# Kernel tuning notes

Hardware: AMD Instinct MI355X
Metric: run time of the kernel (lower is better)

The kernel has to match this reference:

```python
import jax, jax.numpy as jnp
import numpy as np

B, T, H = 4, 2048, 1024
N, D = 16, 64  # heads, key_dim (= value_dim)
SCALE = 1.0 / float(D) ** 0.5


def setup_inputs() -> dict:
    key = jax.random.key(0)
    ks = jax.random.split(key, 10)
    s = 0.02
    return {
        "query": jax.random.normal(ks[0], (B, T, H), jnp.float32),
        "value": jax.random.normal(ks[1], (B, T, H), jnp.float32),
        "Wq": jax.random.normal(ks[2], (N * D, H), jnp.float32) * s,
        "bq": jnp.zeros((N * D,), jnp.float32),
        "Wk": jax.random.normal(ks[3], (N * D, H), jnp.float32) * s,
        "bk": jnp.zeros((N * D,), jnp.float32),
        "Wv": jax.random.normal(ks[4], (N * D, H), jnp.float32) * s,
        "bv": jnp.zeros((N * D,), jnp.float32),
        "Wo": jax.random.normal(ks[5], (H, N * D), jnp.float32) * s,
        "bo": jnp.zeros((H,), jnp.float32),
    }


def reference(query, value, Wq, bq, Wk, bk, Wv, bv, Wo, bo):
    key_in = value  # key=None path: key = value
    q = (query @ Wq.T + bq).reshape(B, -1, N, D)   # [B,T,N,D]
    k = (key_in @ Wk.T + bk).reshape(B, -1, N, D)  # [B,S,N,D]
    v = (value @ Wv.T + bv).reshape(B, -1, N, D)   # [B,S,N,D]
    # scores [T,S,B,N], softmax over S (axis=1), scaled dot-product
    scores = jnp.einsum('btnd,bsnd->tsbn', q, k) * SCALE
    attn = jax.nn.softmax(scores, axis=1)
    # output [B,T,N,D]
    out = jnp.einsum('tsbn,bsnd->btnd', attn, v)
    out = out.reshape(B, T, N * D)
    return out @ Wo.T + bo
```

## Files before the change

### kernel.cpp

```cpp
#include <hip/hip_runtime.h>
#include <cstdint>
#include <cstddef>

typedef unsigned short u16;
typedef __bf16 bf16x8 __attribute__((ext_vector_type(8)));
typedef __bf16 bf16x2 __attribute__((ext_vector_type(2)));
typedef float f32x4 __attribute__((ext_vector_type(4)));
typedef float f32x16 __attribute__((ext_vector_type(16)));

#define B_   4
#define T_   2048
#define H_   1024
#define NH_  16
#define DH_  64
#define M_   (B_ * T_)
#define KDIM 1024
#define QSCALE 0.18033688011112042f

#define BM 128
#define BN 128
#define BK 32

__device__ __forceinline__ u16 f2bf(float f) {
    unsigned u = __float_as_uint(f);
    unsigned r = (u + 0x7fffu + ((u >> 16) & 1u)) >> 16;
    return (u16)r;
}

__device__ __forceinline__ unsigned packbf2(float a, float b) {
    bf16x2 v = { (__bf16)a, (__bf16)b };
    return __builtin_bit_cast(unsigned, v);
}

__device__ __forceinline__ float exp2_fast(float x) {
#if __has_builtin(__builtin_amdgcn_exp2f)
    return __builtin_amdgcn_exp2f(x);
#else
    return exp2f(x);
#endif
}

__device__ __forceinline__ void plswap(unsigned &a, unsigned &b) {
#if __has_builtin(__builtin_amdgcn_permlane32_swap)
    auto r = __builtin_amdgcn_permlane32_swap(a, b, false, false);
    a = (unsigned)r[0]; b = (unsigned)r[1];
#else
    int hi = (threadIdx.x & 32);
    unsigned x = (unsigned)__shfl_xor((int)(hi ? b : a), 32);
    unsigned na = hi ? x : a;
    unsigned nb = hi ? b : x;
    a = na; b = nb;
#endif
}

__device__ __forceinline__ void gload16(const void* g, void* l) {
    __builtin_amdgcn_global_load_lds(
        (const __attribute__((address_space(1))) unsigned int*)g,
        (__attribute__((address_space(3))) unsigned int*)l,
        16, 0, 0);
}

__device__ __forceinline__ f32x16 mfma32(bf16x8 a, bf16x8 b, f32x16 c) {
    return __builtin_amdgcn_mfma_f32_32x32x16_bf16(a, b, c, 0, 0, 0);
}

__global__ __launch_bounds__(256) void f2bf_hex(
    const float* s0, u16* d0, int n0, const float* s1, u16* d1, int n1,
    const float* s2, u16* d2, int n2, const float* s3, u16* d3, int n3,
    const float* s4, u16* d4, int n4j, const float* s5, u16* d5, int n5)
{
    const float* s; u16* d; int n;
    switch (blockIdx.y) {
        case 0: s = s0; d = d0; n = n0; break;
        case 1: s = s1; d = d1; n = n1; break;
        case 2: s = s2; d = d2; n = n2; break;
        case 3: s = s3; d = d3; n = n3; break;
        case 4: s = s4; d = d4; n = n4j; break;
        default: s = s5; d = d5; n = n5; break;
    }
    int i = blockIdx.x * blockDim.x + threadIdx.x;
    int stride = gridDim.x * blockDim.x;
    for (; i < n; i += stride) {
        float4 f = reinterpret_cast<const float4*>(s)[i];
        ushort4 o;
        o.x = f2bf(f.x); o.y = f2bf(f.y); o.z = f2bf(f.z); o.w = f2bf(f.w);
        reinterpret_cast<ushort4*>(d)[i] = o;
    }
}

__device__ __forceinline__ void gemm_core(
    const u16* __restrict__ X, const u16* __restrict__ W,
    const float* __restrict__ bias,
    u16* __restrict__ dst_bf, float* __restrict__ dst_f,
    float scale, int mode, int r0, int c0)
{
    __shared__ u16 lds[17408];
    char* ldsA = (char*)lds;
    char* ldsB = (char*)lds + 8192;

    const int tid = threadIdx.x;
    const int wid = tid >> 6;
    const int l15 = tid & 15;
    const int l4  = (tid & 63) >> 4;
    const int wr = wid >> 1, wc = wid & 1;

    const u16* gA = X + (size_t)(r0 + (tid >> 2)) * KDIM + (tid & 3) * 8;
    const u16* gB = W + (size_t)(c0 + (tid >> 2)) * KDIM + (tid & 3) * 8;
    char* sA0 = ldsA + wid * 1024;
    char* sA1 = ldsA + 4096 + wid * 1024;
    char* sB0 = ldsB + wid * 1024;
    char* sB1 = ldsB + 4096 + wid * 1024;

    f32x4 acc[4][4];
#pragma unroll
    for (int m = 0; m < 4; ++m)
#pragma unroll
        for (int n = 0; n < 4; ++n) acc[m][n] = (f32x4){0.f, 0.f, 0.f, 0.f};

    gload16(gA, sA0); gload16(gA + 64 * KDIM, sA1);
    gload16(gB, sB0); gload16(gB + 64 * KDIM, sB1);

    const int arow = wr * 64 + l15;
    const int brow = wc * 64 + l15;

    for (int kt = 0; kt < KDIM / BK; ++kt) {
        __syncthreads();
        bf16x8 a[4], b[4];
#pragma unroll
        for (int m = 0; m < 4; ++m)
            a[m] = *(const bf16x8*)(ldsA + (arow + m * 16) * 64 + l4 * 16);
#pragma unroll
        for (int n = 0; n < 4; ++n)
            b[n] = *(const bf16x8*)(ldsB + (brow + n * 16) * 64 + l4 * 16);
#pragma unroll
        for (int m = 0; m < 4; ++m)
#pragma unroll
            for (int n = 0; n < 4; ++n)
                acc[m][n] = __builtin_amdgcn_mfma_f32_16x16x32_bf16(a[m], b[n], acc[m][n], 0, 0, 0);
        __syncthreads();
        if (kt + 1 < KDIM / BK) {
            const u16* pa = gA + (kt + 1) * BK;
            const u16* pb = gB + (kt + 1) * BK;
            gload16(pa, sA0); gload16(pa + 64 * KDIM, sA1);
            gload16(pb, sB0); gload16(pb + 64 * KDIM, sB1);
        }
    }

    if (mode == 2) {
#pragma unroll
        for (int m = 0; m < 4; ++m)
#pragma unroll
            for (int n = 0; n < 4; ++n) {
                int cg = c0 + wc * 64 + n * 16 + l15;
                float bv = bias[cg];
                int rg = r0 + wr * 64 + m * 16 + l4 * 4;
#pragma unroll
                for (int j = 0; j < 4; ++j)
                    dst_f[(size_t)(rg + j) * H_ + cg] = acc[m][n][j] + bv;
            }
    } else if (mode == 0) {
        __syncthreads();
        u16 (*ldsR)[136] = (u16(*)[136])lds;
#pragma unroll
        for (int m = 0; m < 4; ++m)
#pragma unroll
            for (int n = 0; n < 4; ++n) {
                int cl = wc * 64 + n * 16 + l15;
                float bv = bias[c0 + cl];
                int rl = wr * 64 + m * 16 + l4 * 4;
#pragma unroll
                for (int j = 0; j < 4; ++j)
                    ldsR[rl + j][cl] = f2bf((acc[m][n][j] + bv) * scale);
            }
        __syncthreads();
        int b2 = r0 >> 11, tb = r0 & (T_ - 1);
#pragma unroll
        for (int it = 0; it < 8; ++it) {
            int id = tid + it * 256;
            int row = id >> 4;
            int ch = id & 15;
            int head = (c0 >> 6) + (ch >> 3);
            int d0 = (ch & 7) * 8;
            uint4 v = *(const uint4*)&ldsR[row][ch * 8];
            *(uint4*)&dst_bf[(((size_t)(b2 * NH_ + head) * T_ + tb + row) << 6) + d0] = v;
        }
    } else {
        __syncthreads();
        u16 (*ldsT)[136] = (u16(*)[136])lds;
#pragma unroll
        for (int m = 0; m < 4; ++m)
#pragma unroll
            for (int n = 0; n < 4; ++n) {
                int cl = wc * 64 + n * 16 + l15;
                float bv = bias[c0 + cl];
                int rl = wr * 64 + m * 16 + l4 * 4;
#pragma unroll
                for (int j = 0; j < 4; ++j)
                    ldsT[cl][rl + j] = f2bf(acc[m][n][j] + bv);
            }
        __syncthreads();
        int b = r0 >> 11, tb = r0 & (T_ - 1);
#pragma unroll
        for (int it = 0; it < 8; ++it) {
            int chunk = tid + it * 256;
            int cl = chunk >> 4;
            int r8 = (chunk & 15) << 3;
            int cg = c0 + cl;
            int head = cg >> 6, d = cg & 63;
            uint4 v = *(const uint4*)&ldsT[cl][r8];
            *(uint4*)&dst_bf[((size_t)((b * NH_ + head) * DH_ + d) * T_) + tb + r8] = v;
        }
    }
}

__global__ __launch_bounds__(256) void gemm_qkv(
    const u16* __restrict__ qbf, const u16* __restrict__ vbf,
    const u16* __restrict__ Wqb, const u16* __restrict__ Wkb, const u16* __restrict__ Wvb,
    const float* __restrict__ bq, const float* __restrict__ bk, const float* __restrict__ bv,
    u16* __restrict__ Qd, u16* __restrict__ Kd, u16* __restrict__ Vtd)
{
    const int orig = blockIdx.y * 24 + blockIdx.x;
    const int swz = (orig & 7) * 192 + (orig >> 3);
    const int bx = swz % 24;
    const int by = swz / 24;
    const int seg = bx >> 3;
    const int r0 = by * BM;
    const int c0 = (bx & 7) * BN;

    if (seg == 0)
        gemm_core(qbf, Wqb, bq, Qd, nullptr, QSCALE, 0, r0, c0);
    else if (seg == 1)
        gemm_core(vbf, Wkb, bk, Kd, nullptr, 1.0f, 0, r0, c0);
    else
        gemm_core(vbf, Wvb, bv, Vtd, nullptr, 1.0f, 1, r0, c0);
}

__global__ __launch_bounds__(256) void gemm_out(
    const u16* __restrict__ AO, const u16* __restrict__ Wob,
    const float* __restrict__ bo, float* __restrict__ out)
{
    const int orig = blockIdx.y * 8 + blockIdx.x;
    const int swz = (orig & 7) * 64 + (orig >> 3);
    const int bx = swz & 7;
    const int by = swz >> 3;
    gemm_core(AO, Wob, bo, nullptr, out, 1.0f, 2, by * BM, bx * BN);
}

#define KVB 64

__global__ __launch_bounds__(256, 2) void attn64(
    const u16* __restrict__ Q, const u16* __restrict__ K,
    const u16* __restrict__ Vt, u16* __restrict__ AO)
{
    __shared__ u16 lds[16384];
    char* const base = (char*)lds;

    const int tid = threadIdx.x;
    const int wid = tid >> 6;
    const int lane = tid & 63;
    const int l31 = lane & 31;
    const int hi = lane >> 5;

    const int orig = blockIdx.y * 8 + blockIdx.x;
    const int swz = (orig & 7) * 64 + (orig >> 3);
    const int bn = swz >> 3;
    const int q0w = (swz & 7) * 256 + wid * 64;
    const int b = bn >> 4, head = bn & 15;

    const u16* Qb = Q + ((size_t)bn * T_ + q0w + l31) * DH_;
    const u16* Kb = K + (size_t)bn * T_ * DH_;
    const u16* Vb = Vt + (size_t)bn * DH_ * T_;

    bf16x8 qfa[4], qfb[4];
#pragma unroll
    for (int c = 0; c < 4; ++c) {
        qfa[c] = *(const bf16x8*)(Qb + c * 16 + hi * 8);
        qfb[c] = *(const bf16x8*)(Qb + 32 * DH_ + c * 16 + hi * 8);
    }

    bf16x8 ones;
#pragma unroll
    for (int e = 0; e < 8; ++e) ones[e] = (__bf16)1.0f;

    f32x16 accO00, accO01, accO10, accO11, La, Lb;
#pragma unroll
    for (int r = 0; r < 16; ++r) {
        accO00[r] = 0.f; accO01[r] = 0.f;
        accO10[r] = 0.f; accO11[r] = 0.f;
        La[r] = 0.f; Lb[r] = 0.f;
    }

    const int srow = tid >> 3;
    const int scsw = (tid & 7) ^ (srow & 7);
    const int rowsw = l31 & 7;

    const u16* kSrc = Kb + (size_t)srow * DH_ + scsw * 8;
    const u16* vSrc = Vb + (size_t)srow * T_ + scsw * 8;

#define STAGE(dK, dV) do { \
    gload16(kSrc,            (dK) + tid * 16); \
    gload16(kSrc + 32 * DH_, (dK) + 4096 + tid * 16); \
    gload16(vSrc,            (dV) + tid * 16); \
    gload16(vSrc + 32 * T_,  (dV) + 4096 + tid * 16); \
    kSrc += KVB * DH_; vSrc += KVB; } while (0)

    char* const kb0 = base;
    char* const vb0 = base + 8192;
    char* const kb1 = base + 16384;
    char* const vb1 = base + 24576;

    auto process = [&](const char* kc, const char* vc) {
        f32x16 sA0, sA1, sB0, sB1;
#pragma unroll
        for (int r = 0; r < 16; ++r) { sA0[r] = 0.f; sA1[r] = 0.f; sB0[r] = 0.f; sB1[r] = 0.f; }
        __builtin_amdgcn_s_setprio(1);
#pragma unroll
        for (int c = 0; c < 4; ++c) {
            const int c16 = ((2 * c + hi) ^ rowsw) * 16;
            bf16x8 k0 = *(const bf16x8*)(kc + l31 * 128 + c16);
            bf16x8 k1 = *(const bf16x8*)(kc + 4096 + l31 * 128 + c16);
            sA0 = mfma32(k0, qfa[c], sA0);
            sA1 = mfma32(k1, qfa[c], sA1);
            sB0 = mfma32(k0, qfb[c], sB0);
            sB1 = mfma32(k1, qfb[c], sB1);
        }
        __builtin_amdgcn_s_setprio(0);

#pragma unroll
        for (int r = 0; r < 16; ++r) {
            sA0[r] = exp2_fast(sA0[r]);
            sA1[r] = exp2_fast(sA1[r]);
            sB0[r] = exp2_fast(sB0[r]);
            sB1[r] = exp2_fast(sB1[r]);
        }

        unsigned w0a[8], w1a[8], w0b[8], w1b[8];
#pragma unroll
        for (int k2 = 0; k2 < 8; ++k2) {
            w0a[k2] = packbf2(sA0[2 * k2], sA0[2 * k2 + 1]);
            w1a[k2] = packbf2(sA1[2 * k2], sA1[2 * k2 + 1]);
            w0b[k2] = packbf2(sB0[2 * k2], sB0[2 * k2 + 1]);
            w1b[k2] = packbf2(sB1[2 * k2], sB1[2 * k2 + 1]);
        }
        plswap(w0a[0], w0a[2]); plswap(w0a[1], w0a[3]);
        plswap(w0a[4], w0a[6]); plswap(w0a[5], w0a[7]);
        plswap(w1a[0], w1a[2]); plswap(w1a[1], w1a[3]);
        plswap(w1a[4], w1a[6]); plswap(w1a[5], w1a[7]);
        plswap(w0b[0], w0b[2]); plswap(w0b[1], w0b[3]);
        plswap(w0b[4], w0b[6]); plswap(w0b[5], w0b[7]);
        plswap(w1b[0], w1b[2]); plswap(w1b[1], w1b[3]);
        plswap(w1b[4], w1b[6]); plswap(w1b[5], w1b[7]);

        __builtin_amdgcn_s_setprio(1);
#pragma unroll
        for (int ks = 0; ks < 4; ++ks) {
            union { unsigned w[4]; bf16x8 v; } pa, pb;
            const unsigned* sa_ = (ks < 2) ? w0a : w1a;
            const unsigned* sb_ = (ks < 2) ? w0b : w1b;
            const int o = (ks & 1) * 4;
            pa.w[0] = sa_[o + 0]; pa.w[1] = sa_[o + 1];
            pa.w[2] = sa_[o + 2]; pa.w[3] = sa_[o + 3];
            pb.w[0] = sb_[o + 0]; pb.w[1] = sb_[o + 1];
            pb.w[2] = sb_[o + 2]; pb.w[3] = sb_[o + 3];
            const int c16 = ((2 * ks + hi) ^ rowsw) * 16;
            bf16x8 v0f = *(const bf16x8*)(vc + l31 * 128 + c16);
            bf16x8 v1f = *(const bf16x8*)(vc + 4096 + l31 * 128 + c16);
            accO00 = mfma32(v0f, pa.v, accO00);
            accO01 = mfma32(v1f, pa.v, accO01);
            accO10 = mfma32(v0f, pb.v, accO10);
            accO11 = mfma32(v1f, pb.v, accO11);
            La = mfma32(ones, pa.v, La);
            Lb = mfma32(ones, pb.v, Lb);
        }
        __builtin_amdgcn_s_setprio(0);
    };

    STAGE(kb0, vb0);
    __syncthreads();

    for (int it = 0; it < T_ / KVB; it += 2) {
        STAGE(kb1, vb1);
        process(kb0, vb0);
        __syncthreads();
        if (it + 2 < T_ / KVB) STAGE(kb0, vb0);
        process(kb1, vb1);
        __syncthreads();
    }

    char* myO = base + wid * 8192;
    float inva = 1.f / La[0];
    float invb = 1.f / Lb[0];
#pragma unroll
    for (int n = 0; n < 2; ++n)
#pragma unroll
        for (int r = 0; r < 16; ++r) {
            int d = n * 32 + (r & 3) + 8 * (r >> 2) + 4 * hi;
            int c16 = (d >> 3) ^ rowsw;
            float va = (n == 0 ? accO00[r] : accO01[r]) * inva;
            float vb2 = (n == 0 ? accO10[r] : accO11[r]) * invb;
            *(u16*)(myO + l31 * 128 + c16 * 16 + (d & 7) * 2) = f2bf(va);
            *(u16*)(myO + (32 + l31) * 128 + c16 * 16 + (d & 7) * 2) = f2bf(vb2);
        }
    asm volatile("s_waitcnt lgkmcnt(0)" ::: "memory");
#pragma unroll
    for (int it = 0; it < 8; ++it) {
        int id = lane + it * 64;
        int row = id >> 3;
        int c = id & 7;
        int c16s = c ^ (row & 7);
        uint4 val = *(const uint4*)(myO + row * 128 + c16s * 16);
        *(uint4*)&AO[(size_t)(b * T_ + q0w + row) * (NH_ * DH_) + head * DH_ + c * 8] = val;
    }
#undef STAGE
}

extern "C" void kernel_launch(void* const* d_in, const int* in_sizes, int n_in,
                              void* d_out, int out_size, void* d_ws, size_t ws_size,
                              hipStream_t stream)
{
    const float* query = (const float*)d_in[0];
    const float* value = (const float*)d_in[1];
    const float* Wq = (const float*)d_in[2];
    const float* bq = (const float*)d_in[3];
    const float* Wk = (const float*)d_in[4];
    const float* bk = (const float*)d_in[5];
    const float* Wv = (const float*)d_in[6];
    const float* bv = (const float*)d_in[7];
    const float* Wo = (const float*)d_in[8];
    const float* bo = (const float*)d_in[9];
    float* out = (float*)d_out;

    u16* ws = (u16*)d_ws;
    const size_t E8M = (size_t)8 << 20;
    u16* qbf = ws;
    u16* vbf = ws + E8M;
    u16* Wqb = ws + 2 * E8M;
    u16* Wkb = Wqb + (1u << 20);
    u16* Wvb = Wkb + (1u << 20);
    u16* Wob = Wvb + (1u << 20);
    u16* Qd  = Wob + (1u << 20);
    u16* Kd  = Qd + E8M;
    u16* Vtd = Kd + E8M;
    u16* AO  = Vtd + E8M;

    const int nBig = (B_ * T_ * H_) / 4;
    const int nW   = (KDIM * KDIM) / 4;
    f2bf_hex<<<dim3(512, 6), 256, 0, stream>>>(
        query, qbf, nBig, value, vbf, nBig,
        Wq, Wqb, nW, Wk, Wkb, nW, Wv, Wvb, nW, Wo, Wob, nW);

    gemm_qkv<<<dim3(24, 64), 256, 0, stream>>>(qbf, vbf, Wqb, Wkb, Wvb,
                                               bq, bk, bv, Qd, Kd, Vtd);

    attn64<<<dim3(8, 64), 256, 0, stream>>>(Qd, Kd, Vtd, AO);

    gemm_out<<<dim3(8, 64), 256, 0, stream>>>(AO, Wob, bo, out);
}
```

Before: 196.8 us.

## Double-buffer GEMM LDS, widen attention KV tile, compute softmax denominator on VALU

The shared GEMM core now keeps two LDS buffers. It prefetches the next K-slice before computing on the current one, which leaves one vmcnt wait plus barrier per step instead of two __syncthreads. The attention kernel loads 128 keys per stage instead of 64, with a wider swizzled V layout and double the LDS (64 KB per block). Each stage is processed as two 64-key halves. The row-sum of probabilities, previously done with extra MFMAs against a vector of ones, is now accumulated in fp32 on the VALU and reduced across the two half-waves at the end, which frees matrix-core cycles at the cost of more VALU adds and higher LDS pressure per block.

```diff
diff --git a/kernel.cpp b/kernel.cpp
--- a/kernel.cpp
+++ b/kernel.cpp
@@ -64,6 +64,10 @@
     return __builtin_amdgcn_mfma_f32_32x32x16_bf16(a, b, c, 0, 0, 0);
 }
 
+__device__ __forceinline__ void wait_barrier() {
+    asm volatile("s_waitcnt vmcnt(0)\n\ts_barrier" ::: "memory");
+}
+
 __global__ __launch_bounds__(256) void f2bf_hex(
     const float* s0, u16* d0, int n0, const float* s1, u16* d1, int n1,
     const float* s2, u16* d2, int n2, const float* s3, u16* d3, int n3,
@@ -95,8 +99,7 @@
     float scale, int mode, int r0, int c0)
 {
     __shared__ u16 lds[17408];
-    char* ldsA = (char*)lds;
-    char* ldsB = (char*)lds + 8192;
+    char* const base = (char*)lds;
 
     const int tid = threadIdx.x;
     const int wid = tid >> 6;
@@ -106,45 +109,45 @@
 
     const u16* gA = X + (size_t)(r0 + (tid >> 2)) * KDIM + (tid & 3) * 8;
     const u16* gB = W + (size_t)(c0 + (tid >> 2)) * KDIM + (tid & 3) * 8;
-    char* sA0 = ldsA + wid * 1024;
-    char* sA1 = ldsA + 4096 + wid * 1024;
-    char* sB0 = ldsB + wid * 1024;
-    char* sB1 = ldsB + 4096 + wid * 1024;
 
     f32x4 acc[4][4];
 #pragma unroll
     for (int m = 0; m < 4; ++m)
 #pragma unroll
         for (int n = 0; n < 4; ++n) acc[m][n] = (f32x4){0.f, 0.f, 0.f, 0.f};
-
-    gload16(gA, sA0); gload16(gA + 64 * KDIM, sA1);
-    gload16(gB, sB0); gload16(gB + 64 * KDIM, sB1);
 
     const int arow = wr * 64 + l15;
     const int brow = wc * 64 + l15;
 
+#define STAGEG(p, kt) do { \
+    const u16* pa_ = gA + (kt) * BK; \
+    const u16* pb_ = gB + (kt) * BK; \
+    char* dA_ = base + (p) * 16384 + wid * 1024; \
+    char* dB_ = dA_ + 8192; \
+    gload16(pa_, dA_); gload16(pa_ + 64 * KDIM, dA_ + 4096); \
+    gload16(pb_, dB_); gload16(pb_ + 64 * KDIM, dB_ + 4096); } while (0)
+
+    STAGEG(0, 0);
+    wait_barrier();
+
     for (int kt = 0; kt < KDIM / BK; ++kt) {
-        __syncthreads();
+        if (kt + 1 < KDIM / BK) STAGEG((kt + 1) & 1, kt + 1);
+        const char* bufp = base + (kt & 1) * 16384;
         bf16x8 a[4], b[4];
 #pragma unroll
         for (int m = 0; m < 4; ++m)
-            a[m] = *(const bf16x8*)(ldsA + (arow + m * 16) * 64 + l4 * 16);
+            a[m] = *(const bf16x8*)(bufp + (arow + m * 16) * 64 + l4 * 16);
 #pragma unroll
         for (int n = 0; n < 4; ++n)
-            b[n] = *(const bf16x8*)(ldsB + (brow + n * 16) * 64 + l4 * 16);
+            b[n] = *(const bf16x8*)(bufp + 8192 + (brow + n * 16) * 64 + l4 * 16);
 #pragma unroll
         for (int m = 0; m < 4; ++m)
 #pragma unroll
             for (int n = 0; n < 4; ++n)
                 acc[m][n] = __builtin_amdgcn_mfma_f32_16x16x32_bf16(a[m], b[n], acc[m][n], 0, 0, 0);
-        __syncthreads();
-        if (kt + 1 < KDIM / BK) {
-            const u16* pa = gA + (kt + 1) * BK;
-            const u16* pb = gB + (kt + 1) * BK;
-            gload16(pa, sA0); gload16(pa + 64 * KDIM, sA1);
-            gload16(pb, sB0); gload16(pb + 64 * KDIM, sB1);
-        }
-    }
+        wait_barrier();
+    }
+#undef STAGEG
 
     if (mode == 2) {
 #pragma unroll
@@ -246,13 +249,13 @@
     gemm_core(AO, Wob, bo, nullptr, out, 1.0f, 2, by * BM, bx * BN);
 }
 
-#define KVB 64
+#define KVB 128
 
 __global__ __launch_bounds__(256, 2) void attn64(
     const u16* __restrict__ Q, const u16* __restrict__ K,
     const u16* __restrict__ Vt, u16* __restrict__ AO)
 {
-    __shared__ u16 lds[16384];
+    __shared__ u16 lds[32768];
     char* const base = (char*)lds;
 
     const int tid = threadIdx.x;
@@ -278,38 +281,37 @@
         qfb[c] = *(const bf16x8*)(Qb + 32 * DH_ + c * 16 + hi * 8);
     }
 
-    bf16x8 ones;
-#pragma unroll
-    for (int e = 0; e < 8; ++e) ones[e] = (__bf16)1.0f;
-
-    f32x16 accO00, accO01, accO10, accO11, La, Lb;
+    f32x16 accO00, accO01, accO10, accO11, Lva, Lvb;
 #pragma unroll
     for (int r = 0; r < 16; ++r) {
         accO00[r] = 0.f; accO01[r] = 0.f;
         accO10[r] = 0.f; accO11[r] = 0.f;
-        La[r] = 0.f; Lb[r] = 0.f;
-    }
-
-    const int srow = tid >> 3;
-    const int scsw = (tid & 7) ^ (srow & 7);
+        Lva[r] = 0.f; Lvb[r] = 0.f;
+    }
+
     const int rowsw = l31 & 7;
 
-    const u16* kSrc = Kb + (size_t)srow * DH_ + scsw * 8;
-    const u16* vSrc = Vb + (size_t)srow * T_ + scsw * 8;
+    const u16* kSrc = Kb + (size_t)(tid >> 3) * DH_ + ((tid & 7) ^ ((tid >> 3) & 7)) * 8;
+    const u16* vSrc = Vb + (size_t)(tid >> 4) * T_ + ((tid & 15) ^ ((tid >> 4) & 15)) * 8;
 
 #define STAGE(dK, dV) do { \
-    gload16(kSrc,            (dK) + tid * 16); \
-    gload16(kSrc + 32 * DH_, (dK) + 4096 + tid * 16); \
-    gload16(vSrc,            (dV) + tid * 16); \
-    gload16(vSrc + 32 * T_,  (dV) + 4096 + tid * 16); \
-    kSrc += KVB * DH_; vSrc += KVB; } while (0)
+    gload16(kSrc,                 (dK) + tid * 16); \
+    gload16(kSrc + 32 * DH_,      (dK) + 4096 + tid * 16); \
+    gload16(kSrc + 64 * DH_,      (dK) + 8192 + tid * 16); \
+    gload16(kSrc + 96 * DH_,      (dK) + 12288 + tid * 16); \
+    gload16(vSrc,                 (dV) + tid * 16); \
+    gload16(vSrc + 16 * T_,       (dV) + 4096 + tid * 16); \
+    gload16(vSrc + 32 * T_,       (dV) + 8192 + tid * 16); \
+    gload16(vSrc + 48 * T_,       (dV) + 12288 + tid * 16); \
+    kSrc += (size_t)KVB * DH_; vSrc += KVB; } while (0)
 
     char* const kb0 = base;
-    char* const vb0 = base + 8192;
-    char* const kb1 = base + 16384;
-    char* const vb1 = base + 24576;
-
-    auto process = [&](const char* kc, const char* vc) {
+    char* const vb0 = base + 16384;
+    char* const kb1 = base + 32768;
+    char* const vb1 = base + 49152;
+
+    auto process = [&](const char* kc, const char* vc, int s) {
+        const char* ks_ = kc + s * 8192;
         f32x16 sA0, sA1, sB0, sB1;
 #pragma unroll
         for (int r = 0; r < 16; ++r) { sA0[r] = 0.f; sA1[r] = 0.f; sB0[r] = 0.f; sB1[r] = 0.f; }
@@ -317,8 +319,8 @@
 #pragma unroll
         for (int c = 0; c < 4; ++c) {
             const int c16 = ((2 * c + hi) ^ rowsw) * 16;
-            bf16x8 k0 = *(const bf16x8*)(kc + l31 * 128 + c16);
-            bf16x8 k1 = *(const bf16x8*)(kc + 4096 + l31 * 128 + c16);
+            bf16x8 k0 = *(const bf16x8*)(ks_ + l31 * 128 + c16);
+            bf16x8 k1 = *(const bf16x8*)(ks_ + 4096 + l31 * 128 + c16);
             sA0 = mfma32(k0, qfa[c], sA0);
             sA1 = mfma32(k1, qfa[c], sA1);
             sB0 = mfma32(k0, qfb[c], sB0);
@@ -332,6 +334,11 @@
             sA1[r] = exp2_fast(sA1[r]);
             sB0[r] = exp2_fast(sB0[r]);
             sB1[r] = exp2_fast(sB1[r]);
+        }
+#pragma unroll
+        for (int r = 0; r < 16; ++r) {
+            Lva[r] += sA0[r] + sA1[r];
+            Lvb[r] += sB0[r] + sB1[r];
         }
 
         unsigned w0a[8], w1a[8], w0b[8], w1b[8];
@@ -362,15 +369,13 @@
             pa.w[2] = sa_[o + 2]; pa.w[3] = sa_[o + 3];
             pb.w[0] = sb_[o + 0]; pb.w[1] = sb_[o + 1];
             pb.w[2] = sb_[o + 2]; pb.w[3] = sb_[o + 3];
-            const int c16 = ((2 * ks + hi) ^ rowsw) * 16;
-            bf16x8 v0f = *(const bf16x8*)(vc + l31 * 128 + c16);
-            bf16x8 v1f = *(const bf16x8*)(vc + 4096 + l31 * 128 + c16);
+            const int cv = ((s * 8 + 2 * ks + hi) ^ (l31 & 15)) * 16;
+            bf16x8 v0f = *(const bf16x8*)(vc + l31 * 256 + cv);
+            bf16x8 v1f = *(const bf16x8*)(vc + (l31 + 32) * 256 + cv);
             accO00 = mfma32(v0f, pa.v, accO00);
             accO01 = mfma32(v1f, pa.v, accO01);
             accO10 = mfma32(v0f, pb.v, accO10);
             accO11 = mfma32(v1f, pb.v, accO11);
-            La = mfma32(ones, pa.v, La);
-            Lb = mfma32(ones, pb.v, Lb);
         }
         __builtin_amdgcn_s_setprio(0);
     };
@@ -380,16 +385,24 @@
 
     for (int it = 0; it < T_ / KVB; it += 2) {
         STAGE(kb1, vb1);
-        process(kb0, vb0);
+        process(kb0, vb0, 0);
+        process(kb0, vb0, 1);
         __syncthreads();
         if (it + 2 < T_ / KVB) STAGE(kb0, vb0);
-        process(kb1, vb1);
-        __syncthreads();
-    }
+        process(kb1, vb1, 0);
+        process(kb1, vb1, 1);
+        __syncthreads();
+    }
+
+    float la = 0.f, lb = 0.f;
+#pragma unroll
+    for (int r = 0; r < 16; ++r) { la += Lva[r]; lb += Lvb[r]; }
+    la += __shfl_xor(la, 32);
+    lb += __shfl_xor(lb, 32);
 
     char* myO = base + wid * 8192;
-    float inva = 1.f / La[0];
-    float invb = 1.f / Lb[0];
+    float inva = 1.f / la;
+    float invb = 1.f / lb;
 #pragma unroll
     for (int n = 0; n < 2; ++n)
 #pragma unroll
```

Measured after the change: 300.9 us. 1.53x slower.

## Double-buffer GEMM LDS tiles and compute softmax denominators with VALU sums

Applied to the files above, without the earlier changes.

The projection GEMM now uses two LDS buffers and issues the next k-tile's global-to-LDS load before computing on the current one. This replaces the old two-barrier-per-iteration scheme with a single explicit waitcnt+barrier per iteration. In the attention kernel, the row-sum denominators are accumulated with scalar VALU adds and one cross-half shuffle instead of two extra MFMAs against a ones vector per k-step. This frees matrix-core cycles and accumulator registers, at the cost of 32 extra VALU adds per tile. The denominator now sums fp32 values rather than bf16-rounded ones, a slight numerical difference.

```diff
diff --git a/kernel.cpp b/kernel.cpp
--- a/kernel.cpp
+++ b/kernel.cpp
@@ -64,6 +64,10 @@
     return __builtin_amdgcn_mfma_f32_32x32x16_bf16(a, b, c, 0, 0, 0);
 }
 
+__device__ __forceinline__ void wait_barrier() {
+    asm volatile("s_waitcnt vmcnt(0) lgkmcnt(0)\n\ts_barrier" ::: "memory");
+}
+
 __global__ __launch_bounds__(256) void f2bf_hex(
     const float* s0, u16* d0, int n0, const float* s1, u16* d1, int n1,
     const float* s2, u16* d2, int n2, const float* s3, u16* d3, int n3,
@@ -95,8 +99,7 @@
     float scale, int mode, int r0, int c0)
 {
     __shared__ u16 lds[17408];
-    char* ldsA = (char*)lds;
-    char* ldsB = (char*)lds + 8192;
+    char* const base = (char*)lds;
 
     const int tid = threadIdx.x;
     const int wid = tid >> 6;
@@ -106,45 +109,45 @@
 
     const u16* gA = X + (size_t)(r0 + (tid >> 2)) * KDIM + (tid & 3) * 8;
     const u16* gB = W + (size_t)(c0 + (tid >> 2)) * KDIM + (tid & 3) * 8;
-    char* sA0 = ldsA + wid * 1024;
-    char* sA1 = ldsA + 4096 + wid * 1024;
-    char* sB0 = ldsB + wid * 1024;
-    char* sB1 = ldsB + 4096 + wid * 1024;
 
     f32x4 acc[4][4];
 #pragma unroll
     for (int m = 0; m < 4; ++m)
 #pragma unroll
         for (int n = 0; n < 4; ++n) acc[m][n] = (f32x4){0.f, 0.f, 0.f, 0.f};
-
-    gload16(gA, sA0); gload16(gA + 64 * KDIM, sA1);
-    gload16(gB, sB0); gload16(gB + 64 * KDIM, sB1);
 
     const int arow = wr * 64 + l15;
     const int brow = wc * 64 + l15;
 
+#define STAGEG(p, kt) do { \
+    const u16* pa_ = gA + (kt) * BK; \
+    const u16* pb_ = gB + (kt) * BK; \
+    char* dA_ = base + (p) * 16384 + wid * 1024; \
+    char* dB_ = dA_ + 8192; \
+    gload16(pa_, dA_); gload16(pa_ + 64 * KDIM, dA_ + 4096); \
+    gload16(pb_, dB_); gload16(pb_ + 64 * KDIM, dB_ + 4096); } while (0)
+
+    STAGEG(0, 0);
+    wait_barrier();
+
     for (int kt = 0; kt < KDIM / BK; ++kt) {
-        __syncthreads();
+        if (kt + 1 < KDIM / BK) STAGEG((kt + 1) & 1, kt + 1);
+        const char* bufp = base + (kt & 1) * 16384;
         bf16x8 a[4], b[4];
 #pragma unroll
         for (int m = 0; m < 4; ++m)
-            a[m] = *(const bf16x8*)(ldsA + (arow + m * 16) * 64 + l4 * 16);
+            a[m] = *(const bf16x8*)(bufp + (arow + m * 16) * 64 + l4 * 16);
 #pragma unroll
         for (int n = 0; n < 4; ++n)
-            b[n] = *(const bf16x8*)(ldsB + (brow + n * 16) * 64 + l4 * 16);
+            b[n] = *(const bf16x8*)(bufp + 8192 + (brow + n * 16) * 64 + l4 * 16);
 #pragma unroll
         for (int m = 0; m < 4; ++m)
 #pragma unroll
             for (int n = 0; n < 4; ++n)
                 acc[m][n] = __builtin_amdgcn_mfma_f32_16x16x32_bf16(a[m], b[n], acc[m][n], 0, 0, 0);
-        __syncthreads();
-        if (kt + 1 < KDIM / BK) {
-            const u16* pa = gA + (kt + 1) * BK;
-            const u16* pb = gB + (kt + 1) * BK;
-            gload16(pa, sA0); gload16(pa + 64 * KDIM, sA1);
-            gload16(pb, sB0); gload16(pb + 64 * KDIM, sB1);
-        }
-    }
+        wait_barrier();
+    }
+#undef STAGEG
 
     if (mode == 2) {
 #pragma unroll
@@ -278,17 +281,13 @@
         qfb[c] = *(const bf16x8*)(Qb + 32 * DH_ + c * 16 + hi * 8);
     }
 
-    bf16x8 ones;
-#pragma unroll
-    for (int e = 0; e < 8; ++e) ones[e] = (__bf16)1.0f;
-
-    f32x16 accO00, accO01, accO10, accO11, La, Lb;
+    f32x16 accO00, accO01, accO10, accO11;
 #pragma unroll
     for (int r = 0; r < 16; ++r) {
         accO00[r] = 0.f; accO01[r] = 0.f;
         accO10[r] = 0.f; accO11[r] = 0.f;
-        La[r] = 0.f; Lb[r] = 0.f;
-    }
+    }
+    float la = 0.f, lb = 0.f;
 
     const int srow = tid >> 3;
     const int scsw = (tid & 7) ^ (srow & 7);
@@ -333,6 +332,13 @@
             sB0[r] = exp2_fast(sB0[r]);
             sB1[r] = exp2_fast(sB1[r]);
         }
+        float ta = 0.f, tb2 = 0.f;
+#pragma unroll
+        for (int r = 0; r < 16; ++r) {
+            ta  += sA0[r] + sA1[r];
+            tb2 += sB0[r] + sB1[r];
+        }
+        la += ta; lb += tb2;
 
         unsigned w0a[8], w1a[8], w0b[8], w1b[8];
 #pragma unroll
@@ -369,8 +375,6 @@
             accO01 = mfma32(v1f, pa.v, accO01);
             accO10 = mfma32(v0f, pb.v, accO10);
             accO11 = mfma32(v1f, pb.v, accO11);
-            La = mfma32(ones, pa.v, La);
-            Lb = mfma32(ones, pb.v, Lb);
         }
         __builtin_amdgcn_s_setprio(0);
     };
@@ -387,9 +391,12 @@
         __syncthreads();
     }
 
+    la += __shfl_xor(la, 32);
+    lb += __shfl_xor(lb, 32);
+
     char* myO = base + wid * 8192;
-    float inva = 1.f / La[0];
-    float invb = 1.f / Lb[0];
+    float inva = 1.f / la;
+    float invb = 1.f / lb;
 #pragma unroll
     for (int n = 0; n < 2; ++n)
 #pragma unroll
```

Result: no change. 194.3 us (-1.3%).
